# Optimization experiments

Measured on AMD Instinct MI355X. Metric: run time of the kernel, lower is better.

Reference implementation:

```python
import jax, jax.numpy as jnp
import numpy as np

# Dims: T timesteps, B batch, C channels, HID expert hidden, E experts, K top-k
T, B, C, HID, E, K, H, W = 4, 8, 256, 1024, 8, 2, 14, 14
EPS = 1e-5       # BatchNorm eps
ALPHA = 4.0      # spikingjelly sigmoid surrogate alpha
V_TH = 1.0       # LIF threshold (spikingjelly default), v_reset = 0.0


@jax.custom_vjp
def spike_fn(u):
    # Heaviside forward, sigmoid-surrogate backward (spikingjelly surrogate.Sigmoid)
    return (u >= 0.0).astype(u.dtype)

def _spike_fwd(u):
    return (u >= 0.0).astype(u.dtype), u

def _spike_bwd(u, g):
    s = jax.nn.sigmoid(ALPHA * u)
    return (g * ALPHA * s * (1.0 - s),)

spike_fn.defvjp(_spike_fwd, _spike_bwd)


def lif(x, tau):
    """MultiStepLIFNode with hard reset (v_reset=0), detach_reset=True.
    x: (T, B, C, H, W) -> spikes of same shape."""
    def step(v, xt):
        h = v + (xt - v) / tau                      # charge
        s = spike_fn(h - V_TH)                      # fire
        v_new = h * (1.0 - jax.lax.stop_gradient(s))  # hard reset, detached spike
        return v_new, s
    _, spikes = jax.lax.scan(step, jnp.zeros_like(x[0]), x)
    return spikes


def conv1x1(x, w, b):
    # x: (T,B,Cin,H,W), w: (Cout,Cin), b: (Cout,) -- 1x1 conv == channel GEMM
    return jnp.einsum('tbchw,oc->tbohw', x, w) + b[None, None, :, None, None]


def bn(x, g, b, m, v, axis):
    # inference-mode BatchNorm with running stats, per-channel on `axis`
    shp = [1] * x.ndim
    shp[axis] = -1
    scale = g.reshape(shp) / jnp.sqrt(v.reshape(shp) + EPS)
    return (x - m.reshape(shp)) * scale + b.reshape(shp)


def expert(x, tau, w1, b1, g1, be1, m1, v1, w2, b2, g2, be2, m2, v2):
    # MS_MLP_Expert.forward: lif -> conv1x1 -> bn -> lif -> conv1x1 -> bn (no residual)
    s1 = lif(x, tau)
    h = bn(conv1x1(s1, w1, b1), g1, be1, m1, v1, axis=2)  # (T,B,HID,H,W)
    s2 = lif(h, tau)
    return bn(conv1x1(s2, w2, b2), g2, be2, m2, v2, axis=2)  # (T,B,C,H,W)


def setup_inputs() -> dict:
    key = jax.random.key(0)
    ks = jax.random.split(key, 16)
    d = {}
    d['x'] = jax.random.normal(ks[0], (T, B, C, H, W), jnp.float32)
    # router (Conv2d(C, E, 1) + BatchNorm2d(E))
    d['router_w'] = jax.random.normal(ks[1], (E, C), jnp.float32) / np.sqrt(C)
    d['router_b'] = jax.random.normal(ks[2], (E,), jnp.float32) * 0.01
    d['rbn_g'] = 1.0 + 0.1 * jax.random.normal(ks[3], (E,), jnp.float32)
    d['rbn_b'] = 0.1 * jax.random.normal(ks[4], (E,), jnp.float32)
    d['rbn_m'] = 0.1 * jax.random.normal(ks[5], (E,), jnp.float32)
    d['rbn_v'] = jax.random.uniform(ks[6], (E,), jnp.float32, 0.5, 1.5)
    # stacked expert params (leading expert axis E)
    d['fc1_w'] = jax.random.normal(ks[7], (E, HID, C), jnp.float32) / np.sqrt(C)
    d['fc1_b'] = 0.01 * jax.random.normal(ks[8], (E, HID), jnp.float32)
    d['bn1_g'] = 1.0 + 0.1 * jax.random.normal(ks[9], (E, HID), jnp.float32)
    d['bn1_b'] = 0.1 * jax.random.normal(ks[10], (E, HID), jnp.float32)
    d['bn1_m'] = 0.1 * jax.random.normal(ks[11], (E, HID), jnp.float32)
    d['bn1_v'] = jax.random.uniform(ks[12], (E, HID), jnp.float32, 0.5, 1.5)
    d['fc2_w'] = jax.random.normal(ks[13], (E, C, HID), jnp.float32) / np.sqrt(HID)
    d['fc2_b'] = 0.01 * jax.random.normal(ks[14], (E, C), jnp.float32)
    d['bn2_g'] = 1.0 + 0.1 * jax.random.normal(ks[15], (E, C), jnp.float32)
    k2 = jax.random.split(jax.random.fold_in(key, 1), 3)
    d['bn2_b'] = 0.1 * jax.random.normal(k2[0], (E, C), jnp.float32)
    d['bn2_m'] = 0.1 * jax.random.normal(k2[1], (E, C), jnp.float32)
    d['bn2_v'] = jax.random.uniform(k2[2], (E, C), jnp.float32, 0.5, 1.5)
    # expert taus: linspace(tau_min=1.5, tau_max=4.0, num_experts)
    d['taus'] = jnp.linspace(1.5, 4.0, E, dtype=jnp.float32)
    return d


def reference(x, router_w, router_b, rbn_g, rbn_b, rbn_m, rbn_v,
              fc1_w, fc1_b, bn1_g, bn1_b, bn1_m, bn1_v,
              fc2_w, fc2_b, bn2_g, bn2_b, bn2_m, bn2_v, taus):
    b_sz = x.shape[1]
    # ---- TemporalRouter ----
    xm = x.mean(axis=0)                                           # (B,C,H,W)
    r = jnp.einsum('bchw,ec->behw', xm, router_w) + router_b[None, :, None, None]
    r = bn(r, rbn_g, rbn_b, rbn_m, rbn_v, axis=1)
    logits = r.mean(axis=(-2, -1))                                # (B,E)
    probs = jax.nn.softmax(logits, axis=-1)
    topw, topi = jax.lax.top_k(probs, K)                          # (B,K)
    topw = topw / topw.sum(axis=-1, keepdims=True)
    # dense combine weights (B,E): top-k entries, 0 elsewhere; detached as in torch
    Wd = jnp.zeros((b_sz, E), x.dtype).at[jnp.arange(b_sz)[:, None], topi].add(topw)
    Wd = jax.lax.stop_gradient(Wd)
    # ---- Experts (dense dispatch: each expert over full batch, masked combine) ----
    outs = jax.vmap(expert, in_axes=(None,) + (0,) * 13)(
        x, taus, fc1_w, fc1_b, bn1_g, bn1_b, bn1_m, bn1_v,
        fc2_w, fc2_b, bn2_g, bn2_b, bn2_m, bn2_v)                 # (E,T,B,C,H,W)
    moe = jnp.einsum('etbchw,be->tbchw', outs, Wd)
    return x + moe
```

## Files before the change

### kernel.cpp

```cpp
#include <hip/hip_runtime.h>
#include <hip/hip_bf16.h>
#include <math.h>

#define T_ 4
#define B_ 8
#define C_ 256
#define HID_ 1024
#define E_ 8
#define K_ 2
#define HW_ 196
#define M_ 784
#define NPAIR_ 16
#define EPS_ 1e-5f

typedef __attribute__((ext_vector_type(8))) short bf16x8;
typedef __attribute__((ext_vector_type(8))) unsigned short u16x8;
typedef __attribute__((ext_vector_type(4))) float f32x4;

__device__ inline unsigned short f2bf(float f){
  union { float f; unsigned u; } v; v.f = f;
  unsigned u = v.u;
  unsigned r = u + 0x7FFFu + ((u >> 16) & 1u);
  return (unsigned short)(r >> 16);
}
__device__ inline float bf2f(unsigned short h){
  union { unsigned u; float f; } v; v.u = ((unsigned)h) << 16;
  return v.f;
}

__global__ __launch_bounds__(256) void wconv_kernel(const float* __restrict__ w,
    unsigned short* __restrict__ hi, unsigned short* __restrict__ lo, int n){
  int i = blockIdx.x * 256 + threadIdx.x;
  if (i >= n) return;
  float f = w[i];
  unsigned short h = f2bf(f);
  hi[i] = h;
  lo[i] = f2bf(f - bf2f(h));
}

__global__ __launch_bounds__(64) void xbar_kernel(const float* __restrict__ x,
                                                  float* __restrict__ xbar){
  int bc = blockIdx.x;
  int l = threadIdx.x;
  float s = 0.f;
  for (int t = 0; t < T_; t++){
    const float* p = x + ((size_t)(t * B_ * C_) + bc) * HW_;
    for (int i = l; i < HW_; i += 64) s += p[i];
  }
  for (int off = 32; off > 0; off >>= 1) s += __shfl_down(s, off, 64);
  if (l == 0) xbar[bc] = s * (1.0f / (T_ * HW_));
}

__global__ __launch_bounds__(64) void router_kernel(const float* __restrict__ xbar,
    const float* __restrict__ rw, const float* __restrict__ rb,
    const float* __restrict__ rg, const float* __restrict__ rbb,
    const float* __restrict__ rm, const float* __restrict__ rv,
    int* __restrict__ sel_e, float* __restrict__ sel_w){
  __shared__ float lg[64];
  const int tid = threadIdx.x;
  const int b = tid >> 3, e = tid & 7;
  float dot = 0.f;
  for (int c = 0; c < C_; c++) dot += xbar[b * C_ + c] * rw[e * C_ + c];
  dot += rb[e];
  float sc = rg[e] / sqrtf(rv[e] + EPS_);
  lg[tid] = (dot - rm[e]) * sc + rbb[e];
  __syncthreads();
  if (e == 0){
    float l[E_], mx = -1e30f;
    for (int i = 0; i < E_; i++){ l[i] = lg[b * 8 + i]; mx = fmaxf(mx, l[i]); }
    float p[E_];
    for (int i = 0; i < E_; i++) p[i] = expf(l[i] - mx);
    int i1 = 0;
    for (int i = 1; i < E_; i++) if (p[i] > p[i1]) i1 = i;
    int i2 = (i1 == 0) ? 1 : 0;
    for (int i = 0; i < E_; i++) if (i != i1 && p[i] > p[i2]) i2 = i;
    float denom = p[i1] + p[i2];
    sel_e[b * 2]     = i1; sel_w[b * 2]     = p[i1] / denom;
    sel_e[b * 2 + 1] = i2; sel_w[b * 2 + 1] = p[i2] / denom;
  }
}

__global__ __launch_bounds__(256) void lif1_kernel(const float* __restrict__ x,
    const int* __restrict__ sel_e, const float* __restrict__ taus,
    unsigned short* __restrict__ s1){
  const int hw = blockIdx.x;
  const int pair = blockIdx.y;
  const int c = threadIdx.x;
  const int b = pair >> 1;
  const float tau = taus[sel_e[pair]];
  float v = 0.f;
  #pragma unroll
  for (int t = 0; t < T_; t++){
    float xv = x[((size_t)(t * B_ + b) * C_ + c) * HW_ + hw];
    float h = v + (xv - v) / tau;
    float s = (h >= 1.0f) ? 1.0f : 0.0f;
    v = h * (1.0f - s);
    s1[((size_t)pair * M_ + hw * 4 + t) * C_ + c] =
        (s > 0.5f) ? (unsigned short)0x3F80 : (unsigned short)0;
  }
}

__global__ __launch_bounds__(256) void g1_kernel(
    const unsigned short* __restrict__ s1,
    const unsigned short* __restrict__ w1h, const unsigned short* __restrict__ w1l,
    const float* __restrict__ fc1_b,
    const float* __restrict__ bn1_g, const float* __restrict__ bn1_b,
    const float* __restrict__ bn1_m, const float* __restrict__ bn1_v,
    const int* __restrict__ sel_e, const float* __restrict__ taus,
    unsigned short* __restrict__ s2)
{
  __shared__ __align__(16) unsigned short lA[64 * 40];
  __shared__ __align__(16) unsigned short lBh[64 * 40];
  __shared__ __align__(16) unsigned short lBl[64 * 40];
  const int nt = blockIdx.x, mt = blockIdx.y, pair = blockIdx.z;
  const int e = sel_e[pair];
  const int m0 = mt * 64, n0 = nt * 64;
  const int tid = threadIdx.x;
  const int row = tid >> 2, seg = tid & 3;
  const int lane = tid & 63, wv = tid >> 6;
  const int koff = (lane >> 4) * 8;
  const unsigned short* s1p = s1 + (size_t)pair * (M_ * C_);
  const unsigned short* bhp = w1h + ((size_t)e * HID_ + n0 + row) * C_ + seg * 8;
  const unsigned short* blp = w1l + ((size_t)e * HID_ + n0 + row) * C_ + seg * 8;
  f32x4 acc[4] = {};
  for (int kk = 0; kk < C_; kk += 32){
    int r = m0 + row;
    u16x8 av = {};
    if (r < M_) av = *(const u16x8*)(s1p + (size_t)r * C_ + kk + seg * 8);
    *(u16x8*)(lA  + row * 40 + seg * 8) = av;
    *(u16x8*)(lBh + row * 40 + seg * 8) = *(const u16x8*)(bhp + kk);
    *(u16x8*)(lBl + row * 40 + seg * 8) = *(const u16x8*)(blp + kk);
    __syncthreads();
    bf16x8 a = *(const bf16x8*)(lA + (wv * 16 + (lane & 15)) * 40 + koff);
    #pragma unroll
    for (int cb = 0; cb < 4; cb++){
      bf16x8 bh = *(const bf16x8*)(lBh + (cb * 16 + (lane & 15)) * 40 + koff);
      bf16x8 bl = *(const bf16x8*)(lBl + (cb * 16 + (lane & 15)) * 40 + koff);
      acc[cb] = __builtin_amdgcn_mfma_f32_16x16x32_bf16(a, bh, acc[cb], 0, 0, 0);
      acc[cb] = __builtin_amdgcn_mfma_f32_16x16x32_bf16(a, bl, acc[cb], 0, 0, 0);
    }
    __syncthreads();
  }
  const float tau = taus[e];
  const int rbase = m0 + wv * 16 + ((lane >> 4) << 2);
  if (rbase < M_){
    #pragma unroll
    for (int cb = 0; cb < 4; cb++){
      int col = n0 + cb * 16 + (lane & 15);
      int pi = e * HID_ + col;
      float sc = bn1_g[pi] / sqrtf(bn1_v[pi] + EPS_);
      float mm = bn1_m[pi], bb = bn1_b[pi], cbias = fc1_b[pi];
      float v = 0.f;
      #pragma unroll
      for (int t = 0; t < 4; t++){
        float z = acc[cb][t] + cbias;
        float hin = (z - mm) * sc + bb;
        float h = v + (hin - v) / tau;
        float s = (h >= 1.0f) ? 1.0f : 0.0f;
        v = h * (1.0f - s);
        s2[((size_t)pair * M_ + rbase + t) * HID_ + col] =
            (s > 0.5f) ? (unsigned short)0x3F80 : (unsigned short)0;
      }
    }
  }
}

__global__ __launch_bounds__(256) void g2_kernel(
    const unsigned short* __restrict__ s2,
    const unsigned short* __restrict__ w2h, const unsigned short* __restrict__ w2l,
    const float* __restrict__ fc2_b,
    const float* __restrict__ bn2_g, const float* __restrict__ bn2_b,
    const float* __restrict__ bn2_m, const float* __restrict__ bn2_v,
    const int* __restrict__ sel_e, const float* __restrict__ sel_w,
    const float* __restrict__ x, float* __restrict__ out)
{
  __shared__ __align__(16) unsigned short lA[64 * 40];
  __shared__ __align__(16) unsigned short lBh[64 * 40];
  __shared__ __align__(16) unsigned short lBl[64 * 40];
  const int nt = blockIdx.x, mt = blockIdx.y, b = blockIdx.z;
  const int m0 = mt * 64, n0 = nt * 64;
  const int tid = threadIdx.x;
  const int row = tid >> 2, seg = tid & 3;
  const int lane = tid & 63, wv = tid >> 6;
  const int koff = (lane >> 4) * 8;
  f32x4 res[4] = {};
  for (int slot = 0; slot < 2; slot++){
    const int pair = b * 2 + slot;
    const int e = sel_e[pair];
    const float wgt = sel_w[pair];
    const unsigned short* s2p = s2 + (size_t)pair * (M_ * HID_);
    const unsigned short* bhp = w2h + ((size_t)e * C_ + n0 + row) * HID_ + seg * 8;
    const unsigned short* blp = w2l + ((size_t)e * C_ + n0 + row) * HID_ + seg * 8;
    f32x4 acc[4] = {};
    for (int kk = 0; kk < HID_; kk += 32){
      int r = m0 + row;
      u16x8 av = {};
      if (r < M_) av = *(const u16x8*)(s2p + (size_t)r * HID_ + kk + seg * 8);
      *(u16x8*)(lA  + row * 40 + seg * 8) = av;
      *(u16x8*)(lBh + row * 40 + seg * 8) = *(const u16x8*)(bhp + kk);
      *(u16x8*)(lBl + row * 40 + seg * 8) = *(const u16x8*)(blp + kk);
      __syncthreads();
      bf16x8 a = *(const bf16x8*)(lA + (wv * 16 + (lane & 15)) * 40 + koff);
      #pragma unroll
      for (int cb = 0; cb < 4; cb++){
        bf16x8 bh = *(const bf16x8*)(lBh + (cb * 16 + (lane & 15)) * 40 + koff);
        bf16x8 bl = *(const bf16x8*)(lBl + (cb * 16 + (lane & 15)) * 40 + koff);
        acc[cb] = __builtin_amdgcn_mfma_f32_16x16x32_bf16(a, bh, acc[cb], 0, 0, 0);
        acc[cb] = __builtin_amdgcn_mfma_f32_16x16x32_bf16(a, bl, acc[cb], 0, 0, 0);
      }
      __syncthreads();
    }
    #pragma unroll
    for (int cb = 0; cb < 4; cb++){
      int col = n0 + cb * 16 + (lane & 15);
      int pi = e * C_ + col;
      float sc = bn2_g[pi] / sqrtf(bn2_v[pi] + EPS_);
      float mm = bn2_m[pi], bb = bn2_b[pi], cbias = fc2_b[pi];
      #pragma unroll
      for (int t = 0; t < 4; t++){
        float z = acc[cb][t] + cbias;
        float y = (z - mm) * sc + bb;
        res[cb][t] += wgt * y;
      }
    }
  }
  const int rbase = m0 + wv * 16 + ((lane >> 4) << 2);
  if (rbase < M_){
    const int hw = rbase >> 2;
    #pragma unroll
    for (int cb = 0; cb < 4; cb++){
      int col = n0 + cb * 16 + (lane & 15);
      #pragma unroll
      for (int t = 0; t < 4; t++){
        size_t oi = ((size_t)(t * B_ + b) * C_ + col) * HW_ + hw;
        out[oi] = x[oi] + res[cb][t];
      }
    }
  }
}

extern "C" void kernel_launch(void* const* d_in, const int* in_sizes, int n_in,
                              void* d_out, int out_size, void* d_ws, size_t ws_size,
                              hipStream_t stream){
  const float* x     = (const float*)d_in[0];
  const float* rw    = (const float*)d_in[1];
  const float* rb    = (const float*)d_in[2];
  const float* rg    = (const float*)d_in[3];
  const float* rbb   = (const float*)d_in[4];
  const float* rm    = (const float*)d_in[5];
  const float* rv    = (const float*)d_in[6];
  const float* fc1_w = (const float*)d_in[7];
  const float* fc1_b = (const float*)d_in[8];
  const float* bn1_g = (const float*)d_in[9];
  const float* bn1_b = (const float*)d_in[10];
  const float* bn1_m = (const float*)d_in[11];
  const float* bn1_v = (const float*)d_in[12];
  const float* fc2_w = (const float*)d_in[13];
  const float* fc2_b = (const float*)d_in[14];
  const float* bn2_g = (const float*)d_in[15];
  const float* bn2_b = (const float*)d_in[16];
  const float* bn2_m = (const float*)d_in[17];
  const float* bn2_v = (const float*)d_in[18];
  const float* taus  = (const float*)d_in[19];
  float* out = (float*)d_out;

  char* ws = (char*)d_ws;
  size_t off = 0;
  auto alloc = [&](size_t bytes) -> char* {
    char* p = ws + off;
    off = (off + bytes + 255) & ~(size_t)255;
    return p;
  };
  const int NW = E_ * HID_ * C_;
  unsigned short* w1h = (unsigned short*)alloc((size_t)NW * 2);
  unsigned short* w1l = (unsigned short*)alloc((size_t)NW * 2);
  unsigned short* w2h = (unsigned short*)alloc((size_t)NW * 2);
  unsigned short* w2l = (unsigned short*)alloc((size_t)NW * 2);
  unsigned short* s1  = (unsigned short*)alloc((size_t)NPAIR_ * M_ * C_ * 2);
  unsigned short* s2  = (unsigned short*)alloc((size_t)NPAIR_ * M_ * HID_ * 2);
  float* xbar  = (float*)alloc(B_ * C_ * 4);
  int*   sel_e = (int*)alloc(NPAIR_ * 4);
  float* sel_w = (float*)alloc(NPAIR_ * 4);
  (void)ws_size; (void)in_sizes; (void)n_in; (void)out_size;

  wconv_kernel<<<(NW + 255) / 256, 256, 0, stream>>>(fc1_w, w1h, w1l, NW);
  wconv_kernel<<<(NW + 255) / 256, 256, 0, stream>>>(fc2_w, w2h, w2l, NW);
  xbar_kernel<<<B_ * C_, 64, 0, stream>>>(x, xbar);
  router_kernel<<<1, 64, 0, stream>>>(xbar, rw, rb, rg, rbb, rm, rv, sel_e, sel_w);
  lif1_kernel<<<dim3(HW_, NPAIR_), 256, 0, stream>>>(x, sel_e, taus, s1);
  g1_kernel<<<dim3(HID_ / 64, (M_ + 63) / 64, NPAIR_), 256, 0, stream>>>(
      s1, w1h, w1l, fc1_b, bn1_g, bn1_b, bn1_m, bn1_v, sel_e, taus, s2);
  g2_kernel<<<dim3(C_ / 64, (M_ + 63) / 64, B_), 256, 0, stream>>>(
      s2, w2h, w2l, fc2_b, bn2_g, bn2_b, bn2_m, bn2_v, sel_e, sel_w, x, out);
}
```

Baseline: 226.8 us.

## Double-buffer GEMM tiles via direct-to-LDS loads and drop fc2 low-part split

Both expert GEMMs now stage A/B tiles with global_load_lds into double-buffered LDS, overlapping the next tile's fetch with MFMA work. The second GEMM keeps only the bf16 high part of fc2 weights, halving its MFMAs and weight traffic at a small accuracy cost. g2 is launched per (batch, slot) pair for more parallelism, and its outputs are summed with x in a separate vectorized combine kernel. Weight conversion is vectorized with float4 loads.

```diff
diff --git a/kernel.cpp b/kernel.cpp
--- a/kernel.cpp
+++ b/kernel.cpp
@@ -7,14 +7,14 @@
 #define C_ 256
 #define HID_ 1024
 #define E_ 8
-#define K_ 2
 #define HW_ 196
 #define M_ 784
 #define NPAIR_ 16
 #define EPS_ 1e-5f
+#define NOUT_ (T_*B_*C_*HW_)
 
 typedef __attribute__((ext_vector_type(8))) short bf16x8;
-typedef __attribute__((ext_vector_type(8))) unsigned short u16x8;
+typedef __attribute__((ext_vector_type(4))) unsigned short u16x4;
 typedef __attribute__((ext_vector_type(4))) float f32x4;
 
 __device__ inline unsigned short f2bf(float f){
@@ -28,14 +28,32 @@
   return v.f;
 }
 
-__global__ __launch_bounds__(256) void wconv_kernel(const float* __restrict__ w,
-    unsigned short* __restrict__ hi, unsigned short* __restrict__ lo, int n){
+__device__ inline void gl16(const void* g, void* l){
+  auto gp = reinterpret_cast<const unsigned int __attribute__((address_space(1)))*>(
+      reinterpret_cast<uintptr_t>(g));
+  auto lp = reinterpret_cast<unsigned int __attribute__((address_space(3)))*>(
+      reinterpret_cast<uintptr_t>(l));
+  __builtin_amdgcn_global_load_lds(gp, lp, 16, 0, 0);
+}
+
+__global__ __launch_bounds__(256) void wconv_hl_kernel(const float* __restrict__ w,
+    unsigned short* __restrict__ hi, unsigned short* __restrict__ lo){
   int i = blockIdx.x * 256 + threadIdx.x;
-  if (i >= n) return;
-  float f = w[i];
-  unsigned short h = f2bf(f);
-  hi[i] = h;
-  lo[i] = f2bf(f - bf2f(h));
+  float4 v = ((const float4*)w)[i];
+  u16x4 h, l;
+  h[0]=f2bf(v.x); l[0]=f2bf(v.x - bf2f(h[0]));
+  h[1]=f2bf(v.y); l[1]=f2bf(v.y - bf2f(h[1]));
+  h[2]=f2bf(v.z); l[2]=f2bf(v.z - bf2f(h[2]));
+  h[3]=f2bf(v.w); l[3]=f2bf(v.w - bf2f(h[3]));
+  ((u16x4*)hi)[i] = h; ((u16x4*)lo)[i] = l;
+}
+__global__ __launch_bounds__(256) void wconv_h_kernel(const float* __restrict__ w,
+    unsigned short* __restrict__ hi){
+  int i = blockIdx.x * 256 + threadIdx.x;
+  float4 v = ((const float4*)w)[i];
+  u16x4 h;
+  h[0]=f2bf(v.x); h[1]=f2bf(v.y); h[2]=f2bf(v.z); h[3]=f2bf(v.w);
+  ((u16x4*)hi)[i] = h;
 }
 
 __global__ __launch_bounds__(64) void xbar_kernel(const float* __restrict__ x,
@@ -109,33 +127,38 @@
     const int* __restrict__ sel_e, const float* __restrict__ taus,
     unsigned short* __restrict__ s2)
 {
-  __shared__ __align__(16) unsigned short lA[64 * 40];
-  __shared__ __align__(16) unsigned short lBh[64 * 40];
-  __shared__ __align__(16) unsigned short lBl[64 * 40];
+  __shared__ __align__(16) unsigned short lA[2][2048];
+  __shared__ __align__(16) unsigned short lBh[2][2048];
+  __shared__ __align__(16) unsigned short lBl[2][2048];
   const int nt = blockIdx.x, mt = blockIdx.y, pair = blockIdx.z;
   const int e = sel_e[pair];
   const int m0 = mt * 64, n0 = nt * 64;
-  const int tid = threadIdx.x;
-  const int row = tid >> 2, seg = tid & 3;
-  const int lane = tid & 63, wv = tid >> 6;
-  const int koff = (lane >> 4) * 8;
-  const unsigned short* s1p = s1 + (size_t)pair * (M_ * C_);
-  const unsigned short* bhp = w1h + ((size_t)e * HID_ + n0 + row) * C_ + seg * 8;
-  const unsigned short* blp = w1l + ((size_t)e * HID_ + n0 + row) * C_ + seg * 8;
+  const int tid = threadIdx.x, lane = tid & 63, wv = tid >> 6;
+  const int l15 = lane & 15, koff = (lane >> 4) * 8;
+  const int srow = wv * 16 + (lane >> 2);
+  const int scol = (lane & 3) * 8;
+  int arow = m0 + srow; if (arow > M_ - 1) arow = M_ - 1;
+  const unsigned short* aG  = s1  + ((size_t)pair * M_ + arow) * C_ + scol;
+  const unsigned short* bhG = w1h + ((size_t)e * HID_ + n0 + srow) * C_ + scol;
+  const unsigned short* blG = w1l + ((size_t)e * HID_ + n0 + srow) * C_ + scol;
+  const int lb = wv * 512;
+  gl16(aG,  &lA[0][lb]);
+  gl16(bhG, &lBh[0][lb]);
+  gl16(blG, &lBl[0][lb]);
+  __syncthreads();
   f32x4 acc[4] = {};
-  for (int kk = 0; kk < C_; kk += 32){
-    int r = m0 + row;
-    u16x8 av = {};
-    if (r < M_) av = *(const u16x8*)(s1p + (size_t)r * C_ + kk + seg * 8);
-    *(u16x8*)(lA  + row * 40 + seg * 8) = av;
-    *(u16x8*)(lBh + row * 40 + seg * 8) = *(const u16x8*)(bhp + kk);
-    *(u16x8*)(lBl + row * 40 + seg * 8) = *(const u16x8*)(blp + kk);
-    __syncthreads();
-    bf16x8 a = *(const bf16x8*)(lA + (wv * 16 + (lane & 15)) * 40 + koff);
+  for (int kk = 0; kk < 8; kk++){
+    const int cur = kk & 1, nxt = cur ^ 1;
+    if (kk < 7){
+      gl16(aG  + (kk + 1) * 32, &lA[nxt][lb]);
+      gl16(bhG + (kk + 1) * 32, &lBh[nxt][lb]);
+      gl16(blG + (kk + 1) * 32, &lBl[nxt][lb]);
+    }
+    bf16x8 a = *(const bf16x8*)(&lA[cur][(wv * 16 + l15) * 32 + koff]);
     #pragma unroll
     for (int cb = 0; cb < 4; cb++){
-      bf16x8 bh = *(const bf16x8*)(lBh + (cb * 16 + (lane & 15)) * 40 + koff);
-      bf16x8 bl = *(const bf16x8*)(lBl + (cb * 16 + (lane & 15)) * 40 + koff);
+      bf16x8 bh = *(const bf16x8*)(&lBh[cur][(cb * 16 + l15) * 32 + koff]);
+      bf16x8 bl = *(const bf16x8*)(&lBl[cur][(cb * 16 + l15) * 32 + koff]);
       acc[cb] = __builtin_amdgcn_mfma_f32_16x16x32_bf16(a, bh, acc[cb], 0, 0, 0);
       acc[cb] = __builtin_amdgcn_mfma_f32_16x16x32_bf16(a, bl, acc[cb], 0, 0, 0);
     }
@@ -146,7 +169,7 @@
   if (rbase < M_){
     #pragma unroll
     for (int cb = 0; cb < 4; cb++){
-      int col = n0 + cb * 16 + (lane & 15);
+      int col = n0 + cb * 16 + l15;
       int pi = e * HID_ + col;
       float sc = bn1_g[pi] / sqrtf(bn1_v[pi] + EPS_);
       float mm = bn1_m[pi], bb = bn1_b[pi], cbias = fc1_b[pi];
@@ -167,76 +190,78 @@
 
 __global__ __launch_bounds__(256) void g2_kernel(
     const unsigned short* __restrict__ s2,
-    const unsigned short* __restrict__ w2h, const unsigned short* __restrict__ w2l,
+    const unsigned short* __restrict__ w2h,
     const float* __restrict__ fc2_b,
     const float* __restrict__ bn2_g, const float* __restrict__ bn2_b,
     const float* __restrict__ bn2_m, const float* __restrict__ bn2_v,
     const int* __restrict__ sel_e, const float* __restrict__ sel_w,
-    const float* __restrict__ x, float* __restrict__ out)
+    float* __restrict__ y)
 {
-  __shared__ __align__(16) unsigned short lA[64 * 40];
-  __shared__ __align__(16) unsigned short lBh[64 * 40];
-  __shared__ __align__(16) unsigned short lBl[64 * 40];
-  const int nt = blockIdx.x, mt = blockIdx.y, b = blockIdx.z;
+  __shared__ __align__(16) unsigned short lA[2][2048];
+  __shared__ __align__(16) unsigned short lBh[2][2048];
+  const int nt = blockIdx.x, mt = blockIdx.y, pair = blockIdx.z;
+  const int e = sel_e[pair];
+  const float wgt = sel_w[pair];
+  const int b = pair >> 1, slot = pair & 1;
   const int m0 = mt * 64, n0 = nt * 64;
-  const int tid = threadIdx.x;
-  const int row = tid >> 2, seg = tid & 3;
-  const int lane = tid & 63, wv = tid >> 6;
-  const int koff = (lane >> 4) * 8;
-  f32x4 res[4] = {};
-  for (int slot = 0; slot < 2; slot++){
-    const int pair = b * 2 + slot;
-    const int e = sel_e[pair];
-    const float wgt = sel_w[pair];
-    const unsigned short* s2p = s2 + (size_t)pair * (M_ * HID_);
-    const unsigned short* bhp = w2h + ((size_t)e * C_ + n0 + row) * HID_ + seg * 8;
-    const unsigned short* blp = w2l + ((size_t)e * C_ + n0 + row) * HID_ + seg * 8;
-    f32x4 acc[4] = {};
-    for (int kk = 0; kk < HID_; kk += 32){
-      int r = m0 + row;
-      u16x8 av = {};
-      if (r < M_) av = *(const u16x8*)(s2p + (size_t)r * HID_ + kk + seg * 8);
-      *(u16x8*)(lA  + row * 40 + seg * 8) = av;
-      *(u16x8*)(lBh + row * 40 + seg * 8) = *(const u16x8*)(bhp + kk);
-      *(u16x8*)(lBl + row * 40 + seg * 8) = *(const u16x8*)(blp + kk);
-      __syncthreads();
-      bf16x8 a = *(const bf16x8*)(lA + (wv * 16 + (lane & 15)) * 40 + koff);
-      #pragma unroll
-      for (int cb = 0; cb < 4; cb++){
-        bf16x8 bh = *(const bf16x8*)(lBh + (cb * 16 + (lane & 15)) * 40 + koff);
-        bf16x8 bl = *(const bf16x8*)(lBl + (cb * 16 + (lane & 15)) * 40 + koff);
-        acc[cb] = __builtin_amdgcn_mfma_f32_16x16x32_bf16(a, bh, acc[cb], 0, 0, 0);
-        acc[cb] = __builtin_amdgcn_mfma_f32_16x16x32_bf16(a, bl, acc[cb], 0, 0, 0);
-      }
-      __syncthreads();
-    }
+  const int tid = threadIdx.x, lane = tid & 63, wv = tid >> 6;
+  const int l15 = lane & 15, koff = (lane >> 4) * 8;
+  const int srow = wv * 16 + (lane >> 2);
+  const int scol = (lane & 3) * 8;
+  int arow = m0 + srow; if (arow > M_ - 1) arow = M_ - 1;
+  const unsigned short* aG  = s2  + ((size_t)pair * M_ + arow) * HID_ + scol;
+  const unsigned short* bhG = w2h + ((size_t)e * C_ + n0 + srow) * HID_ + scol;
+  const int lb = wv * 512;
+  gl16(aG,  &lA[0][lb]);
+  gl16(bhG, &lBh[0][lb]);
+  __syncthreads();
+  f32x4 acc[4] = {};
+  for (int kk = 0; kk < 32; kk++){
+    const int cur = kk & 1, nxt = cur ^ 1;
+    if (kk < 31){
+      gl16(aG  + (kk + 1) * 32, &lA[nxt][lb]);
+      gl16(bhG + (kk + 1) * 32, &lBh[nxt][lb]);
+    }
+    bf16x8 a = *(const bf16x8*)(&lA[cur][(wv * 16 + l15) * 32 + koff]);
     #pragma unroll
     for (int cb = 0; cb < 4; cb++){
-      int col = n0 + cb * 16 + (lane & 15);
+      bf16x8 bh = *(const bf16x8*)(&lBh[cur][(cb * 16 + l15) * 32 + koff]);
+      acc[cb] = __builtin_amdgcn_mfma_f32_16x16x32_bf16(a, bh, acc[cb], 0, 0, 0);
+    }
+    __syncthreads();
+  }
+  const int rbase = m0 + wv * 16 + ((lane >> 4) << 2);
+  if (rbase < M_){
+    const int hw = rbase >> 2;
+    #pragma unroll
+    for (int cb = 0; cb < 4; cb++){
+      int col = n0 + cb * 16 + l15;
       int pi = e * C_ + col;
       float sc = bn2_g[pi] / sqrtf(bn2_v[pi] + EPS_);
       float mm = bn2_m[pi], bb = bn2_b[pi], cbias = fc2_b[pi];
       #pragma unroll
       for (int t = 0; t < 4; t++){
         float z = acc[cb][t] + cbias;
-        float y = (z - mm) * sc + bb;
-        res[cb][t] += wgt * y;
+        float yv = (z - mm) * sc + bb;
+        y[(((size_t)slot * T_ + t) * B_ + b) * (C_ * HW_) + (size_t)col * HW_ + hw] =
+            wgt * yv;
       }
     }
   }
-  const int rbase = m0 + wv * 16 + ((lane >> 4) << 2);
-  if (rbase < M_){
-    const int hw = rbase >> 2;
-    #pragma unroll
-    for (int cb = 0; cb < 4; cb++){
-      int col = n0 + cb * 16 + (lane & 15);
-      #pragma unroll
-      for (int t = 0; t < 4; t++){
-        size_t oi = ((size_t)(t * B_ + b) * C_ + col) * HW_ + hw;
-        out[oi] = x[oi] + res[cb][t];
-      }
-    }
-  }
+}
+
+__global__ __launch_bounds__(256) void combine_kernel(const float* __restrict__ x,
+    const float* __restrict__ y, float* __restrict__ out){
+  int i = blockIdx.x * 256 + threadIdx.x;
+  float4 a  = ((const float4*)x)[i];
+  float4 b0 = ((const float4*)y)[i];
+  float4 b1 = ((const float4*)y)[i + NOUT_ / 4];
+  float4 r;
+  r.x = a.x + b0.x + b1.x;
+  r.y = a.y + b0.y + b1.y;
+  r.z = a.z + b0.z + b1.z;
+  r.w = a.w + b0.w + b1.w;
+  ((float4*)out)[i] = r;
 }
 
 extern "C" void kernel_launch(void* const* d_in, const int* in_sizes, int n_in,
@@ -272,24 +297,25 @@
     return p;
   };
   const int NW = E_ * HID_ * C_;
+  unsigned short* s2  = (unsigned short*)alloc((size_t)NPAIR_ * M_ * HID_ * 2);
+  unsigned short* w2h = (unsigned short*)alloc((size_t)NW * 2);
   unsigned short* w1h = (unsigned short*)alloc((size_t)NW * 2);
   unsigned short* w1l = (unsigned short*)alloc((size_t)NW * 2);
-  unsigned short* w2h = (unsigned short*)alloc((size_t)NW * 2);
-  unsigned short* w2l = (unsigned short*)alloc((size_t)NW * 2);
   unsigned short* s1  = (unsigned short*)alloc((size_t)NPAIR_ * M_ * C_ * 2);
-  unsigned short* s2  = (unsigned short*)alloc((size_t)NPAIR_ * M_ * HID_ * 2);
   float* xbar  = (float*)alloc(B_ * C_ * 4);
   int*   sel_e = (int*)alloc(NPAIR_ * 4);
   float* sel_w = (float*)alloc(NPAIR_ * 4);
+  float* y = (float*)w1h;
   (void)ws_size; (void)in_sizes; (void)n_in; (void)out_size;
 
-  wconv_kernel<<<(NW + 255) / 256, 256, 0, stream>>>(fc1_w, w1h, w1l, NW);
-  wconv_kernel<<<(NW + 255) / 256, 256, 0, stream>>>(fc2_w, w2h, w2l, NW);
+  wconv_hl_kernel<<<NW / 4 / 256, 256, 0, stream>>>(fc1_w, w1h, w1l);
+  wconv_h_kernel <<<NW / 4 / 256, 256, 0, stream>>>(fc2_w, w2h);
   xbar_kernel<<<B_ * C_, 64, 0, stream>>>(x, xbar);
   router_kernel<<<1, 64, 0, stream>>>(xbar, rw, rb, rg, rbb, rm, rv, sel_e, sel_w);
   lif1_kernel<<<dim3(HW_, NPAIR_), 256, 0, stream>>>(x, sel_e, taus, s1);
   g1_kernel<<<dim3(HID_ / 64, (M_ + 63) / 64, NPAIR_), 256, 0, stream>>>(
       s1, w1h, w1l, fc1_b, bn1_g, bn1_b, bn1_m, bn1_v, sel_e, taus, s2);
-  g2_kernel<<<dim3(C_ / 64, (M_ + 63) / 64, B_), 256, 0, stream>>>(
-      s2, w2h, w2l, fc2_b, bn2_g, bn2_b, bn2_m, bn2_v, sel_e, sel_w, x, out);
-}
+  g2_kernel<<<dim3(C_ / 64, (M_ + 63) / 64, NPAIR_), 256, 0, stream>>>(
+      s2, w2h, fc2_b, bn2_g, bn2_b, bn2_m, bn2_v, sel_e, sel_w, y);
+  combine_kernel<<<NOUT_ / 4 / 256, 256, 0, stream>>>(x, y, out);
+}
```

Measured after the change: 196.9 us. 13.2% less time.
